# Optimization experiments

Measured on AMD Instinct MI355X. Metric: run time of the kernel, lower is better.

The kernel has to match this reference:

```python
import jax, jax.numpy as jnp
import numpy as np

N, T0, T1, C = 65536, 128, 64, 16
MIN_NEAR = 0.05


def _searchsorted(a, v):
    # batched right-side searchsorted over last dim
    return jax.vmap(lambda aa, vv: jnp.searchsorted(aa, vv, side='right'))(a, v)


def contract(x):
    # MERF-style contraction, x: [..., 3]
    ax = jnp.abs(x)
    mag = jnp.max(ax, axis=-1, keepdims=True)              # [..., 1]
    idx = jnp.argmax(ax, axis=-1)                          # [...]
    oh = jnp.arange(x.shape[-1]) == idx[..., None]         # one-hot of max axis
    inv = 1.0 / mag
    scale = jnp.where(oh, (2.0 - inv) * inv, inv)
    return jnp.where(mag < 1.0, x, x * scale)


def sample_pdf(bins, weights, T):
    # bins: [N, T0+1], weights: [N, T0] -> new bins [N, T]
    n, t0 = weights.shape
    w = weights + 0.01
    pdf = w / jnp.sum(w, -1, keepdims=True)
    cdf = jnp.minimum(jnp.cumsum(pdf, -1), 1.0)
    cdf = jnp.concatenate([jnp.zeros_like(cdf[..., :1]), cdf], -1)  # [N, T0+1]
    u = jnp.linspace(0.5 / T, 1.0 - 0.5 / T, T, dtype=bins.dtype)
    u = jnp.broadcast_to(u, (n, T))
    inds = _searchsorted(cdf, u)
    below = jnp.clip(inds - 1, 0, t0)
    above = jnp.clip(inds, 0, t0)
    g = lambda a, i: jnp.take_along_axis(a, i, axis=-1)
    cdf0, cdf1 = g(cdf, below), g(cdf, above)
    b0, b1 = g(bins, below), g(bins, above)
    t = jnp.clip(jnp.nan_to_num((u - cdf0) / (cdf1 - cdf0)), 0.0, 1.0)
    return b0 + t * (b1 - b0)


def compute_weights(real_bins, sigmas):
    deltas = real_bins[..., 1:] - real_bins[..., :-1]
    ds = deltas * sigmas
    alphas = 1.0 - jnp.exp(-ds)
    trans = jnp.exp(-jnp.concatenate(
        [jnp.zeros_like(ds[..., :1]), jnp.cumsum(ds[..., :-1], -1)], -1))
    return jnp.nan_to_num(alphas * trans)


def loss_interlevel(t0, w0, t1, w1):
    cw1 = jnp.concatenate([jnp.zeros_like(w1[..., :1]), jnp.cumsum(w1, -1)], -1)
    hi_clip = w1.shape[-1] - 1
    inds_lo = jnp.clip(_searchsorted(t1[..., :-1], t0[..., :-1]) - 1, 0, hi_clip)
    inds_hi = jnp.clip(_searchsorted(t1[..., 1:], t0[..., 1:]), 0, hi_clip)
    cw1_lo = jnp.take_along_axis(cw1[..., :-1], inds_lo, axis=-1)
    cw1_hi = jnp.take_along_axis(cw1[..., 1:], inds_hi, axis=-1)
    w = cw1_hi - cw1_lo
    return jnp.maximum(w0 - w, 0.0) ** 2 / (w0 + 1e-8)


def eff_distloss(w, m, interval):
    # efficient O(T) distortion loss (torch_efficient_distloss)
    loss_uni = (1.0 / 3.0) * jnp.mean(jnp.sum(interval * w ** 2, -1))
    wm = w * m
    w_cs = jnp.cumsum(w, -1)
    wm_cs = jnp.cumsum(wm, -1)
    loss_bi = 2.0 * jnp.mean(jnp.sum(
        wm[..., 1:] * w_cs[..., :-1] - w[..., 1:] * wm_cs[..., :-1], -1))
    return loss_uni + loss_bi


def setup_inputs():
    key = jax.random.key(0)
    ks = jax.random.split(key, 8)
    rays_o = 0.1 * jax.random.normal(ks[0], (N, 3), jnp.float32)
    rd = jax.random.normal(ks[1], (N, 3), jnp.float32)
    rays_d = rd / jnp.linalg.norm(rd, axis=-1, keepdims=True)
    aabb = jnp.array([-2.0, -2.0, -2.0, 2.0, 2.0, 2.0], jnp.float32)
    sigmas_coarse = 5.0 * jax.random.uniform(ks[2], (N, T0), jnp.float32)
    sigmas_fine = 5.0 * jax.random.uniform(ks[3], (N, T1), jnp.float32)
    colors = jax.random.uniform(ks[4], (N, T1, C), jnp.float32)
    w_view = 0.1 * jax.random.normal(ks[5], (C, 3), jnp.float32)
    b_view = jnp.zeros((3,), jnp.float32)
    return dict(rays_o=rays_o, rays_d=rays_d, aabb=aabb,
                sigmas_coarse=sigmas_coarse, sigmas_fine=sigmas_fine,
                colors=colors, w_view=w_view, b_view=b_view)


def reference(rays_o, rays_d, aabb, sigmas_coarse, sigmas_fine, colors, w_view, b_view):
    # near/far from aabb
    tmin = (aabb[:3] - rays_o) / (rays_d + 1e-15)
    tmax = (aabb[3:] - rays_o) / (rays_d + 1e-15)
    near = jnp.max(jnp.minimum(tmin, tmax), -1, keepdims=True)
    far = jnp.min(jnp.maximum(tmin, tmax), -1, keepdims=True)
    bad = far < near
    near = jnp.maximum(jnp.where(bad, 1e9, near), MIN_NEAR)
    far = jnp.where(bad, 1e9, far)

    spacing = lambda x: jnp.where(x < 1.0, x / 2.0, 1.0 - 1.0 / (2.0 * x))
    spacing_inv = lambda x: jnp.where(x < 0.5, 2.0 * x, 1.0 / (2.0 - 2.0 * x))
    s_near, s_far = spacing(near), spacing(far)

    # coarse (proposal) level: uniform bins in warped space
    bins0 = jnp.broadcast_to(jnp.linspace(0.0, 1.0, T0 + 1, dtype=rays_o.dtype), (N, T0 + 1))
    real_bins0 = spacing_inv(s_near * (1.0 - bins0) + s_far * bins0)
    weights0 = compute_weights(real_bins0, sigmas_coarse)

    # fine level: inverse-CDF sampling (detached in original)
    bins1 = sample_pdf(jax.lax.stop_gradient(bins0),
                       jax.lax.stop_gradient(weights0), T1 + 1)
    real_bins1 = spacing_inv(s_near * (1.0 - bins1) + s_far * bins1)
    rays_t = 0.5 * (real_bins1[..., 1:] + real_bins1[..., :-1])      # [N, T1]
    xyzs = rays_o[:, None, :] + rays_d[:, None, :] * rays_t[..., None]
    xyzs = contract(xyzs)                                            # [N, T1, 3]
    weights1 = compute_weights(real_bins1, sigmas_fine)

    weights_sum = jnp.sum(weights1, -1)                              # [N]
    depth = jnp.sum(weights1 * rays_t, -1)                           # [N]
    f_image = jnp.sum(weights1[..., None] * colors, -2)              # [N, C]
    image = jax.nn.sigmoid(f_image @ w_view + b_view)                # [N, 3]
    image = image + (1.0 - weights_sum)[:, None] * 1.0               # bg_color = 1
    f_xyz = jnp.sum(weights1[..., None] * xyzs, -2)                  # [N, 3]

    prop_loss = jnp.mean(loss_interlevel(
        jax.lax.stop_gradient(bins1), jax.lax.stop_gradient(weights1),
        bins0, weights0))
    intervals = bins1[..., 1:] - bins1[..., :-1]
    mids = bins1[..., :-1] + intervals / 2.0
    dist_loss = eff_distloss(weights1, mids, intervals)

    return image, depth, f_xyz, prop_loss, dist_loss
```

## Files before the change

kernel.cpp:

```cpp
#include <hip/hip_runtime.h>
#include <math.h>

#define NRAYS 65536
#define T0N 128
#define T1N 64
#define CN 16
#define RPB 4
#define NBLK (NRAYS / RPB)

#define IMG_OFF   0
#define DEPTH_OFF (NRAYS * 3)
#define FXYZ_OFF  (NRAYS * 4)
#define PROP_OFF  (NRAYS * 7)
#define DIST_OFF  (NRAYS * 7 + 1)

__device__ __forceinline__ float wave_sum(float x) {
#pragma unroll
  for (int off = 1; off < 64; off <<= 1) x += __shfl_xor(x, off, 64);
  return x;
}

__device__ __forceinline__ float scan_incl(float x, int lane) {
#pragma unroll
  for (int off = 1; off < 64; off <<= 1) {
    float y = __shfl_up(x, off, 64);
    if (lane >= off) x += y;
  }
  return x;
}

__device__ __forceinline__ void wave_lds_sync() {
  __builtin_amdgcn_wave_barrier();
  __builtin_amdgcn_fence(__ATOMIC_ACQ_REL, "workgroup");
  __builtin_amdgcn_wave_barrier();
}

__device__ __forceinline__ float spacing_fn(float x) {
  return (x < 1.0f) ? (x * 0.5f) : (1.0f - 1.0f / (2.0f * x));
}
__device__ __forceinline__ float spacing_inv_fn(float x) {
  return (x < 0.5f) ? (2.0f * x) : (1.0f / (2.0f - 2.0f * x));
}

__device__ __forceinline__ int ss_right(const float* a, int n, float v) {
  int lo = 0, hi = n;
  while (lo < hi) {
    int m = (lo + hi) >> 1;
    if (a[m] <= v) lo = m + 1; else hi = m;
  }
  return lo;
}

__global__ void __launch_bounds__(256) nerf_main(
    const float* __restrict__ rays_o, const float* __restrict__ rays_d,
    const float* __restrict__ aabb, const float* __restrict__ sig_c,
    const float* __restrict__ sig_f, const float* __restrict__ colors,
    const float* __restrict__ w_view, const float* __restrict__ b_view,
    float* __restrict__ out, float* __restrict__ ws_partials, int use_atomic) {
  __shared__ float s_cdf[RPB][130];
  __shared__ float s_bins1[RPB][65];
  __shared__ float s_cw1[RPB][65];
  __shared__ float s_scal[RPB][2];

  const int wv = threadIdx.x >> 6;
  const int lane = threadIdx.x & 63;
  const int ray = blockIdx.x * RPB + wv;

  const int tg = lane >> 2, cg = lane & 3;
  const float4* col4 = (const float4*)(colors + (size_t)ray * (T1N * CN));
  const float4 cva = col4[(tg + 0) * 4 + cg];
  const float4 cvb = col4[(tg + 16) * 4 + cg];
  const float4 cvc = col4[(tg + 32) * 4 + cg];
  const float4 cvd = col4[(tg + 48) * 4 + cg];
  const float2 sg = ((const float2*)sig_c)[ray * 64 + lane];
  const float sgf = sig_f[ray * 64 + lane];

  float ro[3], rd[3];
#pragma unroll
  for (int c = 0; c < 3; ++c) { ro[c] = rays_o[ray * 3 + c]; rd[c] = rays_d[ray * 3 + c]; }
  float near = -3.0e38f, far = 3.0e38f;
#pragma unroll
  for (int c = 0; c < 3; ++c) {
    float dd = rd[c] + 1e-15f;
    float ta = (aabb[c] - ro[c]) / dd;
    float tb = (aabb[c + 3] - ro[c]) / dd;
    near = fmaxf(near, fminf(ta, tb));
    far = fminf(far, fmaxf(ta, tb));
  }
  if (far < near) { near = 1e9f; far = 1e9f; }
  near = fmaxf(near, 0.05f);
  const float s_near = spacing_fn(near), s_far = spacing_fn(far);

  const int i0 = 2 * lane, i1 = 2 * lane + 1;
  const float b_a = (float)i0 * (1.0f / 128.0f);
  const float b_b = (float)i1 * (1.0f / 128.0f);
  const float b_c = (float)(i1 + 1) * (1.0f / 128.0f);
  const float rb_a = spacing_inv_fn(s_near * (1.0f - b_a) + s_far * b_a);
  const float rb_b = spacing_inv_fn(s_near * (1.0f - b_b) + s_far * b_b);
  const float rb_c = spacing_inv_fn(s_near * (1.0f - b_c) + s_far * b_c);
  const float ds0 = (rb_b - rb_a) * sg.x;
  const float ds1 = (rb_c - rb_b) * sg.y;
  const float pr = ds0 + ds1;
  const float Spr = scan_incl(pr, lane);
  const float E0 = Spr - pr;
  const float e0 = __expf(-E0);
  const float ed0 = __expf(-ds0);
  float w00 = (1.0f - ed0) * e0;
  float w01 = (1.0f - __expf(-ds1)) * (e0 * ed0);
  if (w00 != w00) w00 = 0.0f;
  if (w01 != w01) w01 = 0.0f;

  const float wp0 = w00 + 0.01f, wp1 = w01 + 0.01f;
  const float S2 = scan_incl(wp0 + wp1, lane);
  const float tot = __shfl(S2, 63, 64);
  const float rt = 1.0f / tot;
  s_cdf[wv][i0 + 1] = fminf((S2 - wp1) * rt, 1.0f);
  s_cdf[wv][i1 + 1] = fminf(S2 * rt, 1.0f);
  if (lane == 0) s_cdf[wv][0] = 0.0f;
  wave_lds_sync();

  auto sample_one = [&](int j) -> float {
    const float u = ((float)j + 0.5f) * (1.0f / 65.0f);
    int inds = ss_right(&s_cdf[wv][0], 129, u);
    int below = max(min(inds - 1, 128), 0);
    int above = min(inds, 128);
    float c0 = s_cdf[wv][below], c1 = s_cdf[wv][above];
    float b0 = (float)below * (1.0f / 128.0f);
    float b1 = (float)above * (1.0f / 128.0f);
    float t = (u - c0) / (c1 - c0);
    t = fminf(fmaxf(t, 0.0f), 1.0f);
    float bvv = b0 + t * (b1 - b0);
    s_bins1[wv][j] = bvv;
    return bvv;
  };
  const float bv = sample_one(lane);
  float bv64 = 0.0f;
  if (lane == 63) bv64 = sample_one(64);
  float bvn = __shfl_down(bv, 1, 64);
  if (lane == 63) bvn = bv64;

  const float rbl  = spacing_inv_fn(s_near * (1.0f - bv)  + s_far * bv);
  const float rbl1 = spacing_inv_fn(s_near * (1.0f - bvn) + s_far * bvn);
  const float dsf = (rbl1 - rbl) * sgf;
  const float Sf = scan_incl(dsf, lane);
  float w1 = (1.0f - __expf(-dsf)) * __expf(-(Sf - dsf));
  if (w1 != w1) w1 = 0.0f;
  const float tmid = 0.5f * (rbl + rbl1);

  float px = ro[0] + rd[0] * tmid;
  float py = ro[1] + rd[1] * tmid;
  float pz = ro[2] + rd[2] * tmid;
  float cx = px, cy = py, cz = pz;
  {
    float ax = fabsf(px), ay = fabsf(py), az = fabsf(pz);
    float mag = fmaxf(ax, fmaxf(ay, az));
    if (mag >= 1.0f) {
      float inv = 1.0f / mag;
      float so = (2.0f - inv) * inv;
      int idx = (ax >= ay && ax >= az) ? 0 : ((ay >= az) ? 1 : 2);
      cx = px * (idx == 0 ? so : inv);
      cy = py * (idx == 1 ? so : inv);
      cz = pz * (idx == 2 ? so : inv);
    }
  }

  const float Scw = scan_incl(w1, lane);
  const float wsum = __shfl(Scw, 63, 64);
  const float depth = wave_sum(w1 * tmid);
  const float fx = wave_sum(w1 * cx);
  const float fy = wave_sum(w1 * cy);
  const float fz = wave_sum(w1 * cz);
  s_cw1[wv][lane + 1] = Scw;
  if (lane == 0) s_cw1[wv][0] = 0.0f;

  const float interval = bvn - bv;
  const float mid = bv + interval * 0.5f;
  const float wm = w1 * mid;
  const float Swm = scan_incl(wm, lane);
  const float dl = (1.0f / 3.0f) * (interval * w1 * w1) +
                   2.0f * (wm * (Scw - w1) - w1 * (Swm - wm));
  const float dist_part = wave_sum(dl);
  wave_lds_sync();

  float prop_lane = 0.0f;
  {
    const float* b1p = &s_bins1[wv][0];
    const float* cwp = &s_cw1[wv][0];
#pragma unroll
    for (int k = 0; k < 2; ++k) {
      int i = 2 * lane + k;
      float w0v = (k == 0) ? w00 : w01;
      float vlo = (float)i * (1.0f / 128.0f);
      float vhi = (float)(i + 1) * (1.0f / 128.0f);
      int ilo = max(min(ss_right(b1p, 64, vlo) - 1, 63), 0);
      int ihi = min(ss_right(b1p + 1, 64, vhi), 63);
      float wint = cwp[ihi + 1] - cwp[ilo];
      float diff = fmaxf(w0v - wint, 0.0f);
      prop_lane += diff * diff / (w0v + 1e-8f);
    }
  }
  const float prop_part = wave_sum(prop_lane);

  float a0, a1, a2, a3;
  {
    const float wv0 = __shfl(w1, tg, 64);
    const float wv1 = __shfl(w1, tg + 16, 64);
    const float wv2 = __shfl(w1, tg + 32, 64);
    const float wv3 = __shfl(w1, tg + 48, 64);
    a0 = fmaf(wv0, cva.x, fmaf(wv1, cvb.x, fmaf(wv2, cvc.x, wv3 * cvd.x)));
    a1 = fmaf(wv0, cva.y, fmaf(wv1, cvb.y, fmaf(wv2, cvc.y, wv3 * cvd.y)));
    a2 = fmaf(wv0, cva.z, fmaf(wv1, cvb.z, fmaf(wv2, cvc.z, wv3 * cvd.z)));
    a3 = fmaf(wv0, cva.w, fmaf(wv1, cvb.w, fmaf(wv2, cvc.w, wv3 * cvd.w)));
#pragma unroll
    for (int m = 4; m < 64; m <<= 1) {
      a0 += __shfl_xor(a0, m, 64);
      a1 += __shfl_xor(a1, m, 64);
      a2 += __shfl_xor(a2, m, 64);
      a3 += __shfl_xor(a3, m, 64);
    }
  }
  float acc0 = 0.f, acc1 = 0.f, acc2 = 0.f;
  {
    const int ch = cg * 4;
    const float* wvp = w_view + ch * 3;
    acc0 = fmaf(a0, wvp[0], fmaf(a1, wvp[3], fmaf(a2, wvp[6], a3 * wvp[9])));
    acc1 = fmaf(a0, wvp[1], fmaf(a1, wvp[4], fmaf(a2, wvp[7], a3 * wvp[10])));
    acc2 = fmaf(a0, wvp[2], fmaf(a1, wvp[5], fmaf(a2, wvp[8], a3 * wvp[11])));
#pragma unroll
    for (int m = 1; m < 4; m <<= 1) {
      acc0 += __shfl_xor(acc0, m, 64);
      acc1 += __shfl_xor(acc1, m, 64);
      acc2 += __shfl_xor(acc2, m, 64);
    }
  }

  if (lane < 3) {
    float acc = (lane == 0) ? acc0 : ((lane == 1) ? acc1 : acc2);
    acc += b_view[lane];
    out[IMG_OFF + ray * 3 + lane] = 1.0f / (1.0f + __expf(-acc)) + (1.0f - wsum);
    out[FXYZ_OFF + ray * 3 + lane] = (lane == 0) ? fx : ((lane == 1) ? fy : fz);
  }
  if (lane == 0) {
    out[DEPTH_OFF + ray] = depth;
    s_scal[wv][0] = prop_part;
    s_scal[wv][1] = dist_part;
  }
  __syncthreads();
  if (threadIdx.x == 0) {
    float P = s_scal[0][0] + s_scal[1][0] + s_scal[2][0] + s_scal[3][0];
    float D = s_scal[0][1] + s_scal[1][1] + s_scal[2][1] + s_scal[3][1];
    if (use_atomic) {
      atomicAdd(out + PROP_OFF, P * (1.0f / ((float)NRAYS * 128.0f)));
      atomicAdd(out + DIST_OFF, D * (1.0f / (float)NRAYS));
    } else {
      ws_partials[blockIdx.x] = P;
      ws_partials[NBLK + blockIdx.x] = D;
    }
  }
}

__global__ void __launch_bounds__(256) reduce_partials(const float* __restrict__ ws,
                                                       float* __restrict__ out) {
  const float4* w4 = (const float4*)ws;
  float p = 0.0f, d = 0.0f;
  for (int i = threadIdx.x; i < NBLK / 4; i += 256) {
    float4 a = w4[i];
    p += (a.x + a.y) + (a.z + a.w);
    float4 b = w4[NBLK / 4 + i];
    d += (b.x + b.y) + (b.z + b.w);
  }
  p = wave_sum(p);
  d = wave_sum(d);
  __shared__ float sp[4], sd[4];
  const int wv = threadIdx.x >> 6, lane = threadIdx.x & 63;
  if (lane == 0) { sp[wv] = p; sd[wv] = d; }
  __syncthreads();
  if (threadIdx.x == 0) {
    float P = sp[0] + sp[1] + sp[2] + sp[3];
    float D = sd[0] + sd[1] + sd[2] + sd[3];
    out[PROP_OFF] = P * (1.0f / ((float)NRAYS * 128.0f));
    out[DIST_OFF] = D * (1.0f / (float)NRAYS);
  }
}

extern "C" void kernel_launch(void* const* d_in, const int* in_sizes, int n_in,
                              void* d_out, int out_size, void* d_ws, size_t ws_size,
                              hipStream_t stream) {
  const float* rays_o = (const float*)d_in[0];
  const float* rays_d = (const float*)d_in[1];
  const float* aabb = (const float*)d_in[2];
  const float* sig_c = (const float*)d_in[3];
  const float* sig_f = (const float*)d_in[4];
  const float* colors = (const float*)d_in[5];
  const float* w_view = (const float*)d_in[6];
  const float* b_view = (const float*)d_in[7];
  float* out = (float*)d_out;
  float* wsf = (float*)d_ws;

  const bool use_ws = (ws_size >= (size_t)(2 * NBLK) * sizeof(float)) && (wsf != nullptr);
  if (!use_ws) {
    hipMemsetAsync(out + PROP_OFF, 0, 2 * sizeof(float), stream);
  }
  nerf_main<<<NBLK, 256, 0, stream>>>(rays_o, rays_d, aabb, sig_c, sig_f, colors,
                                      w_view, b_view, out, wsf, use_ws ? 0 : 1);
  if (use_ws) reduce_partials<<<1, 256, 0, stream>>>(wsf, out);
}
```

Baseline: 410.7 us.

## Use DPP wave scans/reductions and branchless padded searches in NeRF kernel

Replaces shuffle-based wave scans and butterfly reductions with DPP row-shift and row-broadcast sequences, and uses readlane for totals. Results are taken from the upper lanes (48-52), where the partial reductions finish. The variable-length binary searches over the CDF and bins become fixed-depth branchless counts, which requires padding the shared arrays with sentinel values. The aim is fewer cross-lane ds_bpermute/LDS round trips and less divergence, at the cost of more shared memory and reliance on the DPP broadcast semantics being correct.

```diff
diff --git a/kernel.cpp b/kernel.cpp
--- a/kernel.cpp
+++ b/kernel.cpp
@@ -14,19 +14,34 @@
 #define PROP_OFF  (NRAYS * 7)
 #define DIST_OFF  (NRAYS * 7 + 1)
 
-__device__ __forceinline__ float wave_sum(float x) {
-#pragma unroll
-  for (int off = 1; off < 64; off <<= 1) x += __shfl_xor(x, off, 64);
+template <int CTRL, int RM, int BM, bool BC>
+__device__ __forceinline__ float dpp_add(float x) {
+  int t = __builtin_amdgcn_update_dpp(0, __float_as_int(x), CTRL, RM, BM, BC);
+  return x + __int_as_float(t);
+}
+
+__device__ __forceinline__ float scan_incl(float x) {
+  x = dpp_add<0x111, 0xF, 0xF, true>(x);
+  x = dpp_add<0x112, 0xF, 0xF, true>(x);
+  x = dpp_add<0x114, 0xF, 0xF, true>(x);
+  x = dpp_add<0x118, 0xF, 0xF, true>(x);
+  x = dpp_add<0x142, 0xA, 0xF, false>(x);
+  x = dpp_add<0x143, 0xC, 0xF, false>(x);
   return x;
 }
 
-__device__ __forceinline__ float scan_incl(float x, int lane) {
-#pragma unroll
-  for (int off = 1; off < 64; off <<= 1) {
-    float y = __shfl_up(x, off, 64);
-    if (lane >= off) x += y;
-  }
+__device__ __forceinline__ float reduce_hi(float x) {
+  x = dpp_add<0xB1, 0xF, 0xF, true>(x);
+  x = dpp_add<0x4E, 0xF, 0xF, true>(x);
+  x = dpp_add<0x141, 0xF, 0xF, true>(x);
+  x = dpp_add<0x140, 0xF, 0xF, true>(x);
+  x = dpp_add<0x142, 0xA, 0xF, false>(x);
+  x = dpp_add<0x143, 0xC, 0xF, false>(x);
   return x;
+}
+
+__device__ __forceinline__ float rl63(float x) {
+  return __int_as_float(__builtin_amdgcn_readlane(__float_as_int(x), 63));
 }
 
 __device__ __forceinline__ void wave_lds_sync() {
@@ -42,13 +57,12 @@
   return (x < 0.5f) ? (2.0f * x) : (1.0f / (2.0f - 2.0f * x));
 }
 
-__device__ __forceinline__ int ss_right(const float* a, int n, float v) {
-  int lo = 0, hi = n;
-  while (lo < hi) {
-    int m = (lo + hi) >> 1;
-    if (a[m] <= v) lo = m + 1; else hi = m;
-  }
-  return lo;
+template <int W0>
+__device__ __forceinline__ int count_le(const float* a, float v) {
+  int pos = 0;
+#pragma unroll
+  for (int w = W0; w > 0; w >>= 1) pos += (a[pos + w - 1] <= v) ? w : 0;
+  return pos;
 }
 
 __global__ void __launch_bounds__(256) nerf_main(
@@ -57,8 +71,8 @@
     const float* __restrict__ sig_f, const float* __restrict__ colors,
     const float* __restrict__ w_view, const float* __restrict__ b_view,
     float* __restrict__ out, float* __restrict__ ws_partials, int use_atomic) {
-  __shared__ float s_cdf[RPB][130];
-  __shared__ float s_bins1[RPB][65];
+  __shared__ float s_cdf[RPB][256];
+  __shared__ float s_bins1[RPB][129];
   __shared__ float s_cw1[RPB][65];
   __shared__ float s_scal[RPB][2];
 
@@ -100,9 +114,8 @@
   const float rb_c = spacing_inv_fn(s_near * (1.0f - b_c) + s_far * b_c);
   const float ds0 = (rb_b - rb_a) * sg.x;
   const float ds1 = (rb_c - rb_b) * sg.y;
-  const float pr = ds0 + ds1;
-  const float Spr = scan_incl(pr, lane);
-  const float E0 = Spr - pr;
+  const float Spr = scan_incl(ds0 + ds1);
+  const float E0 = Spr - (ds0 + ds1);
   const float e0 = __expf(-E0);
   const float ed0 = __expf(-ds0);
   float w00 = (1.0f - ed0) * e0;
@@ -111,38 +124,37 @@
   if (w01 != w01) w01 = 0.0f;
 
   const float wp0 = w00 + 0.01f, wp1 = w01 + 0.01f;
-  const float S2 = scan_incl(wp0 + wp1, lane);
-  const float tot = __shfl(S2, 63, 64);
-  const float rt = 1.0f / tot;
+  const float S2 = scan_incl(wp0 + wp1);
+  const float rt = 1.0f / rl63(S2);
   s_cdf[wv][i0 + 1] = fminf((S2 - wp1) * rt, 1.0f);
   s_cdf[wv][i1 + 1] = fminf(S2 * rt, 1.0f);
   if (lane == 0) s_cdf[wv][0] = 0.0f;
+  s_cdf[wv][129 + lane] = 2.0f;
+  if (lane < 63) s_cdf[wv][193 + lane] = 2.0f;
   wave_lds_sync();
 
   auto sample_one = [&](int j) -> float {
     const float u = ((float)j + 0.5f) * (1.0f / 65.0f);
-    int inds = ss_right(&s_cdf[wv][0], 129, u);
-    int below = max(min(inds - 1, 128), 0);
-    int above = min(inds, 128);
-    float c0 = s_cdf[wv][below], c1 = s_cdf[wv][above];
-    float b0 = (float)below * (1.0f / 128.0f);
-    float b1 = (float)above * (1.0f / 128.0f);
+    const int c = count_le<128>(&s_cdf[wv][0], u);
+    const float c0 = s_cdf[wv][c - 1], c1 = s_cdf[wv][c];
+    const float b0 = (float)(c - 1) * (1.0f / 128.0f);
     float t = (u - c0) / (c1 - c0);
     t = fminf(fmaxf(t, 0.0f), 1.0f);
-    float bvv = b0 + t * (b1 - b0);
+    const float bvv = b0 + t * (1.0f / 128.0f);
     s_bins1[wv][j] = bvv;
     return bvv;
   };
   const float bv = sample_one(lane);
   float bv64 = 0.0f;
   if (lane == 63) bv64 = sample_one(64);
+  s_bins1[wv][65 + lane] = 2.0f;
   float bvn = __shfl_down(bv, 1, 64);
   if (lane == 63) bvn = bv64;
 
   const float rbl  = spacing_inv_fn(s_near * (1.0f - bv)  + s_far * bv);
   const float rbl1 = spacing_inv_fn(s_near * (1.0f - bvn) + s_far * bvn);
   const float dsf = (rbl1 - rbl) * sgf;
-  const float Sf = scan_incl(dsf, lane);
+  const float Sf = scan_incl(dsf);
   float w1 = (1.0f - __expf(-dsf)) * __expf(-(Sf - dsf));
   if (w1 != w1) w1 = 0.0f;
   const float tmid = 0.5f * (rbl + rbl1);
@@ -164,22 +176,22 @@
     }
   }
 
-  const float Scw = scan_incl(w1, lane);
-  const float wsum = __shfl(Scw, 63, 64);
-  const float depth = wave_sum(w1 * tmid);
-  const float fx = wave_sum(w1 * cx);
-  const float fy = wave_sum(w1 * cy);
-  const float fz = wave_sum(w1 * cz);
+  const float Scw = scan_incl(w1);
+  const float wsum = rl63(Scw);
+  const float depth_h = reduce_hi(w1 * tmid);
+  const float fx_h = reduce_hi(w1 * cx);
+  const float fy_h = reduce_hi(w1 * cy);
+  const float fz_h = reduce_hi(w1 * cz);
   s_cw1[wv][lane + 1] = Scw;
   if (lane == 0) s_cw1[wv][0] = 0.0f;
 
   const float interval = bvn - bv;
   const float mid = bv + interval * 0.5f;
   const float wm = w1 * mid;
-  const float Swm = scan_incl(wm, lane);
+  const float Swm = scan_incl(wm);
   const float dl = (1.0f / 3.0f) * (interval * w1 * w1) +
                    2.0f * (wm * (Scw - w1) - w1 * (Swm - wm));
-  const float dist_part = wave_sum(dl);
+  const float dist_h = reduce_hi(dl);
   wave_lds_sync();
 
   float prop_lane = 0.0f;
@@ -192,59 +204,40 @@
       float w0v = (k == 0) ? w00 : w01;
       float vlo = (float)i * (1.0f / 128.0f);
       float vhi = (float)(i + 1) * (1.0f / 128.0f);
-      int ilo = max(min(ss_right(b1p, 64, vlo) - 1, 63), 0);
-      int ihi = min(ss_right(b1p + 1, 64, vhi), 63);
+      int ilo = max(min(count_le<64>(b1p, vlo) - 1, 63), 0);
+      int ihi = min(count_le<64>(b1p + 1, vhi), 63);
       float wint = cwp[ihi + 1] - cwp[ilo];
       float diff = fmaxf(w0v - wint, 0.0f);
       prop_lane += diff * diff / (w0v + 1e-8f);
     }
   }
-  const float prop_part = wave_sum(prop_lane);
-
-  float a0, a1, a2, a3;
+  const float prop_h = reduce_hi(prop_lane);
+
+  float acc0, acc1, acc2;
   {
     const float wv0 = __shfl(w1, tg, 64);
     const float wv1 = __shfl(w1, tg + 16, 64);
     const float wv2 = __shfl(w1, tg + 32, 64);
     const float wv3 = __shfl(w1, tg + 48, 64);
-    a0 = fmaf(wv0, cva.x, fmaf(wv1, cvb.x, fmaf(wv2, cvc.x, wv3 * cvd.x)));
-    a1 = fmaf(wv0, cva.y, fmaf(wv1, cvb.y, fmaf(wv2, cvc.y, wv3 * cvd.y)));
-    a2 = fmaf(wv0, cva.z, fmaf(wv1, cvb.z, fmaf(wv2, cvc.z, wv3 * cvd.z)));
-    a3 = fmaf(wv0, cva.w, fmaf(wv1, cvb.w, fmaf(wv2, cvc.w, wv3 * cvd.w)));
-#pragma unroll
-    for (int m = 4; m < 64; m <<= 1) {
-      a0 += __shfl_xor(a0, m, 64);
-      a1 += __shfl_xor(a1, m, 64);
-      a2 += __shfl_xor(a2, m, 64);
-      a3 += __shfl_xor(a3, m, 64);
-    }
-  }
-  float acc0 = 0.f, acc1 = 0.f, acc2 = 0.f;
-  {
-    const int ch = cg * 4;
-    const float* wvp = w_view + ch * 3;
-    acc0 = fmaf(a0, wvp[0], fmaf(a1, wvp[3], fmaf(a2, wvp[6], a3 * wvp[9])));
-    acc1 = fmaf(a0, wvp[1], fmaf(a1, wvp[4], fmaf(a2, wvp[7], a3 * wvp[10])));
-    acc2 = fmaf(a0, wvp[2], fmaf(a1, wvp[5], fmaf(a2, wvp[8], a3 * wvp[11])));
-#pragma unroll
-    for (int m = 1; m < 4; m <<= 1) {
-      acc0 += __shfl_xor(acc0, m, 64);
-      acc1 += __shfl_xor(acc1, m, 64);
-      acc2 += __shfl_xor(acc2, m, 64);
-    }
-  }
-
-  if (lane < 3) {
-    float acc = (lane == 0) ? acc0 : ((lane == 1) ? acc1 : acc2);
-    acc += b_view[lane];
-    out[IMG_OFF + ray * 3 + lane] = 1.0f / (1.0f + __expf(-acc)) + (1.0f - wsum);
-    out[FXYZ_OFF + ray * 3 + lane] = (lane == 0) ? fx : ((lane == 1) ? fy : fz);
-  }
-  if (lane == 0) {
-    out[DEPTH_OFF + ray] = depth;
-    s_scal[wv][0] = prop_part;
-    s_scal[wv][1] = dist_part;
-  }
+    const float a0 = fmaf(wv0, cva.x, fmaf(wv1, cvb.x, fmaf(wv2, cvc.x, wv3 * cvd.x)));
+    const float a1 = fmaf(wv0, cva.y, fmaf(wv1, cvb.y, fmaf(wv2, cvc.y, wv3 * cvd.y)));
+    const float a2 = fmaf(wv0, cva.z, fmaf(wv1, cvb.z, fmaf(wv2, cvc.z, wv3 * cvd.z)));
+    const float a3 = fmaf(wv0, cva.w, fmaf(wv1, cvb.w, fmaf(wv2, cvc.w, wv3 * cvd.w)));
+    const float* wvp = w_view + cg * 12;
+    acc0 = reduce_hi(fmaf(a0, wvp[0], fmaf(a1, wvp[3], fmaf(a2, wvp[6], a3 * wvp[9]))));
+    acc1 = reduce_hi(fmaf(a0, wvp[1], fmaf(a1, wvp[4], fmaf(a2, wvp[7], a3 * wvp[10]))));
+    acc2 = reduce_hi(fmaf(a0, wvp[2], fmaf(a1, wvp[5], fmaf(a2, wvp[8], a3 * wvp[11]))));
+  }
+
+  if (lane >= 48 && lane < 51) {
+    const int j = lane - 48;
+    float acc = (j == 0) ? acc0 : ((j == 1) ? acc1 : acc2);
+    acc += b_view[j];
+    out[IMG_OFF + ray * 3 + j] = 1.0f / (1.0f + __expf(-acc)) + (1.0f - wsum);
+    out[FXYZ_OFF + ray * 3 + j] = (j == 0) ? fx_h : ((j == 1) ? fy_h : fz_h);
+  }
+  if (lane == 51) out[DEPTH_OFF + ray] = depth_h;
+  if (lane == 52) { s_scal[wv][0] = prop_h; s_scal[wv][1] = dist_h; }
   __syncthreads();
   if (threadIdx.x == 0) {
     float P = s_scal[0][0] + s_scal[1][0] + s_scal[2][0] + s_scal[3][0];
@@ -259,6 +252,12 @@
   }
 }
 
+__device__ __forceinline__ float wave_sum_shfl(float x) {
+#pragma unroll
+  for (int off = 1; off < 64; off <<= 1) x += __shfl_xor(x, off, 64);
+  return x;
+}
+
 __global__ void __launch_bounds__(256) reduce_partials(const float* __restrict__ ws,
                                                        float* __restrict__ out) {
   const float4* w4 = (const float4*)ws;
@@ -269,8 +268,8 @@
     float4 b = w4[NBLK / 4 + i];
     d += (b.x + b.y) + (b.z + b.w);
   }
-  p = wave_sum(p);
-  d = wave_sum(d);
+  p = wave_sum_shfl(p);
+  d = wave_sum_shfl(d);
   __shared__ float sp[4], sd[4];
   const int wv = threadIdx.x >> 6, lane = threadIdx.x & 63;
   if (lane == 0) { sp[wv] = p; sd[wv] = d; }
```

Measured after the change: 411.4 us. Within noise of the previous version (+0.2%).
